# Performance work log

Measured on AMD Instinct MI355X. Metric: run time of the kernel, lower is better.

Reference implementation:

```python
import jax, jax.numpy as jnp
import numpy as np

IN_SIZE = 1024
HID = 2048
OUT = 1024
M_STEPS = 100   # max extra ponder steps -> up to M_STEPS+1 total steps
EPS = 0.01


def setup_inputs() -> dict:
    key = jax.random.key(0)
    ks = jax.random.split(key, 11)
    inv = 1.0 / np.sqrt(HID)

    def unif(k, shape, scale):
        return jax.random.uniform(k, shape, jnp.float32, -scale, scale)

    return {
        "x": jax.random.normal(ks[0], (IN_SIZE,), jnp.float32),
        "h0": jax.random.normal(ks[1], (HID,), jnp.float32) * 0.1,
        "c0": jax.random.normal(ks[2], (HID,), jnp.float32) * 0.1,
        "W_ih": unif(ks[3], (4 * HID, 1 + IN_SIZE), inv),
        "b_ih": unif(ks[4], (4 * HID,), inv),
        "W_hh": unif(ks[5], (4 * HID, HID), inv),
        "b_hh": unif(ks[6], (4 * HID,), inv),
        "w_halt": unif(ks[7], (HID,), inv),
        "b_halt": jnp.ones((1,), jnp.float32),  # fc_halt.bias = 1.0 per source
        "W_out": unif(ks[8], (OUT, HID), inv),
        "b_out": unif(ks[9], (OUT,), inv),
    }


def reference(x, h0, c0, W_ih, b_ih, W_hh, b_hh, w_halt, b_halt, W_out, b_out):
    # Input contribution is constant across steps except the prepended halt flag
    # (1 on first step, 0 after). Precompute it once.
    ih_x = W_ih[:, 1:] @ x + b_ih + b_hh      # (4H,)
    w_flag = W_ih[:, 0]                        # (4H,)

    def step(carry, flag):
        h, c = carry
        gates = ih_x + flag * w_flag + W_hh @ h  # (4H,)
        i, f, g, o = jnp.split(gates, 4)
        i = jax.nn.sigmoid(i)
        f = jax.nn.sigmoid(f)
        g = jnp.tanh(g)
        o = jax.nn.sigmoid(o)
        c = f * c + i * g
        h = o * jnp.tanh(c)
        return (h, c), (h, c)

    flags = jnp.concatenate(
        [jnp.ones((1,), x.dtype), jnp.zeros((M_STEPS,), x.dtype)])
    _, (H, C) = jax.lax.scan(step, (h0, c0), flags)  # (M+1, HID) each

    p = jax.nn.sigmoid(H @ w_halt + b_halt[0])       # (M+1,) halting probs
    csum = jnp.cumsum(p)
    halted = csum >= 1.0 - EPS
    # n = first step where cumulative halt prob crosses threshold, capped at M
    n = jnp.where(jnp.any(halted), jnp.argmax(halted), M_STEPS)
    # remainder r = 1 - sum(p[:n]); csum[n] - p[n] == sum(p[:n])
    r = 1.0 - jnp.where(n > 0, csum[n] - p[n], 0.0)

    idx = jnp.arange(M_STEPS + 1)
    w = jnp.where(idx < n, p, jnp.where(idx == n, r, 0.0))  # (M+1,)

    outputs = H @ W_out.T + b_out                    # (M+1, OUT)
    output = w @ outputs                             # (OUT,) weights sum to 1
    h_out = w @ H                                    # (HID,)
    c_out = w @ C                                    # (HID,)
    ponder = n.astype(x.dtype) + 1.0 + r
    return output, (h_out, c_out), ponder
```

## Files before the change

kernel.cpp:

```cpp
#include <hip/hip_runtime.h>


#define HID    2048
#define INS    1024
#define OUTS   1024
#define MSTEPS 100
#define NBLK   256
#define NTHR   512
#define NWAVE  8
#define JPB    8
#define RPB    32
#define SLOTF  16

typedef unsigned long long u64;
typedef unsigned int u32;

__device__ __forceinline__ float wave_allreduce(float v) {
    #pragma unroll
    for (int off = 32; off > 0; off >>= 1)
        v += __shfl_xor(v, off, 64);
    return v;
}

__device__ __forceinline__ u32 bf16_2(float a, float b) {
    u32 ua = __float_as_uint(a), ub = __float_as_uint(b);
    ua = (ua + 0x7fffu + ((ua >> 16) & 1u)) >> 16;
    ub = (ub + 0x7fffu + ((ub >> 16) & 1u)) >> 16;
    return ua | (ub << 16);
}
__device__ __forceinline__ float blo(u32 u) { return __uint_as_float(u << 16); }
__device__ __forceinline__ float bhi(u32 u) { return __uint_as_float(u & 0xffff0000u); }

__device__ __forceinline__ u64 pack_tag(unsigned tag, float v) {
    return ((u64)tag << 32) | (u64)__float_as_uint(v);
}
__device__ __forceinline__ u64 aload(const u64* p) {
    return __hip_atomic_load(p, __ATOMIC_RELAXED, __HIP_MEMORY_SCOPE_AGENT);
}
__device__ __forceinline__ void astore(u64* p, u64 v) {
    __hip_atomic_store(p, v, __ATOMIC_RELAXED, __HIP_MEMORY_SCOPE_AGENT);
}


__global__ __launch_bounds__(NTHR, 2) void alstm_kernel(
    const float* __restrict__ x,      const float* __restrict__ h0,
    const float* __restrict__ c0,     const float* __restrict__ W_ih,
    const float* __restrict__ b_ih,   const float* __restrict__ W_hh,
    const float* __restrict__ b_hh,   const float* __restrict__ w_halt,
    const float* __restrict__ b_halt, const float* __restrict__ W_out,
    const float* __restrict__ b_out,  float* __restrict__ out,
    float* __restrict__ ws)
{
    const int b    = blockIdx.x;
    const int tid  = threadIdx.x;
    const int wave = tid >> 6;
    const int lane = tid & 63;

    float* arrive = ws;
    float* mail   = ws + NBLK * SLOTF;
    float* hbuf0  = ws + 2 * NBLK * SLOTF;
    float* hbuf1  = hbuf0 + HID;
    float* hbar_g = hbuf0 + 2 * HID;

    __shared__ u32   whh_u[RPB * 1024];
    __shared__ u32   hpk[HID / 2];
    __shared__ float x_lds[INS];
    __shared__ float hbar_lds[HID];
    __shared__ float gate_lds[RPB];
    __shared__ float ihx_lds[RPB];
    __shared__ float wflag_lds[RPB];
    __shared__ float red_lds[4];
    __shared__ float bcast_lds;
    __shared__ float psum[NWAVE];

    const float bh = b_halt[0];
    const int j_own = b * JPB + tid;

    const int lr0   = 4 * wave;
    const int rbase = (lr0 >> 3) * HID + b * JPB + (lr0 & 7);

    #define SYNC_ROUND(tag_, part_, dot_) do {                                 \
        if (tid == 0) {                                                        \
            __threadfence();           \
            astore((u64*)(arrive + SLOTF * b), pack_tag((tag_), (part_)));     \
        }                                                                      \
        if (b == 0) {                                                          \
            float pf = 0.f;                                                    \
            if (tid < NBLK) {                                                  \
                u64 v;                                                         \
                do { v = aload((u64*)(arrive + SLOTF * tid)); }                \
                while ((unsigned)(v >> 32) != (unsigned)(tag_));               \
                pf = __uint_as_float((unsigned)v);                             \
            }                                                                  \
            float s = wave_allreduce(pf);                                      \
            if (lane == 0 && wave < 4) red_lds[wave] = s;                      \
            __syncthreads();                                                   \
            if (tid == 0)                                                      \
                bcast_lds = red_lds[0] + red_lds[1] + red_lds[2] + red_lds[3]; \
            __syncthreads();                                                   \
            if (tid < NBLK)                                                    \
                astore((u64*)(mail + SLOTF * tid), pack_tag((tag_), bcast_lds)); \
        }                                                                      \
        if (tid == 0) {                                                        \
            u64 v;                                                             \
            do { v = aload((u64*)(mail + SLOTF * b)); }                        \
            while ((unsigned)(v >> 32) != (unsigned)(tag_));                   \
            bcast_lds = __uint_as_float((unsigned)v);                          \
            __threadfence();        \
        }                                                                      \
        __syncthreads();                                                       \
        (dot_) = bcast_lds;                                                    \
    } while (0)

    ((float2*)x_lds)[tid] = ((const float2*)x)[tid];
    {
        float4 v = ((const float4*)h0)[tid];
        hpk[2 * tid]     = bf16_2(v.x, v.y);
        hpk[2 * tid + 1] = bf16_2(v.z, v.w);
    }
    __syncthreads();

    {
        float4 st[4][8];
        #pragma unroll
        for (int rr = 0; rr < 4; ++rr) {
            const float4* src = (const float4*)(W_hh + (size_t)(rbase + rr) * HID);
            #pragma unroll
            for (int m = 0; m < 8; ++m) st[rr][m] = src[lane + 64 * m];
        }
        __builtin_amdgcn_sched_barrier(0);
        #pragma unroll
        for (int rr = 0; rr < 4; ++rr) {
            u32* dst = whh_u + (lr0 + rr) * (HID / 2);
            #pragma unroll
            for (int m = 0; m < 8; ++m) {
                dst[2 * (lane + 64 * m)]     = bf16_2(st[rr][m].x, st[rr][m].y);
                dst[2 * (lane + 64 * m) + 1] = bf16_2(st[rr][m].z, st[rr][m].w);
            }
        }
    }

    float a0 = 0.f, a1 = 0.f, a2 = 0.f, a3 = 0.f;
    {
        const float*  wr_[4];
        const float4* wv_[4];
        int p0_[4];
        #pragma unroll
        for (int rr = 0; rr < 4; ++rr) {
            const int lr = lr0 + rr;
            const int r  = (lr >> 3) * HID + b * JPB + (lr & 7);
            wr_[rr] = W_ih + (size_t)r * (INS + 1) + 1;
            p0_[rr] = (4 - ((r + 1) & 3)) & 3;
            wv_[rr] = (const float4*)(wr_[rr] + p0_[rr]);
        }
        float bsum = 0.f, wflg = 0.f;
        if (lane < 4) {
            const int lr = lr0 + lane;
            const int r  = (lr >> 3) * HID + b * JPB + (lr & 7);
            bsum = b_ih[r] + b_hh[r];
            wflg = W_ih[(size_t)r * (INS + 1)];
        }
        #pragma unroll
        for (int ii = 0; ii < 4; ++ii) {
            const int i = lane + 64 * ii;
            if (i < 255) {
                #pragma unroll
                for (int rr = 0; rr < 4; ++rr) {
                    float4 w4 = wv_[rr][i];
                    const int k = p0_[rr] + 4 * i;
                    float s = w4.x * x_lds[k]     + w4.y * x_lds[k + 1]
                            + w4.z * x_lds[k + 2] + w4.w * x_lds[k + 3];
                    if      (rr == 0) a0 += s;
                    else if (rr == 1) a1 += s;
                    else if (rr == 2) a2 += s;
                    else              a3 += s;
                }
            }
        }
        if (lane < 4) {
            #pragma unroll
            for (int rr = 0; rr < 4; ++rr) {
                const int p0 = p0_[rr];
                const int e  = (lane < p0) ? lane : 1020 + lane;
                float s = wr_[rr][e] * x_lds[e];
                if      (rr == 0) a0 += s;
                else if (rr == 1) a1 += s;
                else if (rr == 2) a2 += s;
                else              a3 += s;
            }
        }
        a0 = wave_allreduce(a0);
        a1 = wave_allreduce(a1);
        a2 = wave_allreduce(a2);
        a3 = wave_allreduce(a3);
        if (lane < 4) {
            float myacc = (lane == 0) ? a0 : (lane == 1) ? a1 : (lane == 2) ? a2 : a3;
            ihx_lds[lr0 + lane]   = myacc + bsum;
            wflag_lds[lr0 + lane] = wflg;
        }
    }

    float c_reg = 0.f, h_reg = 0.f, hbar = 0.f, cbar = 0.f;
    if (tid < JPB) c_reg = c0[j_own];

    float csum = 0.f, r_halt = 0.f;
    int   n_halt = 0;
    for (int t = 0; t <= MSTEPS; ++t) {
        {
            const uint4* hp = (const uint4*)hpk;
            float g0 = 0.f, g1 = 0.f, g2 = 0.f, g3 = 0.f;
            #pragma unroll
            for (int m = 0; m < 4; ++m) {
                uint4 hu = hp[lane + 64 * m];
                float h0a = blo(hu.x), h1a = bhi(hu.x);
                float h2a = blo(hu.y), h3a = bhi(hu.y);
                float h4a = blo(hu.z), h5a = bhi(hu.z);
                float h6a = blo(hu.w), h7a = bhi(hu.w);
                #pragma unroll
                for (int rr = 0; rr < 4; ++rr) {
                    const uint4* wp = (const uint4*)(whh_u + (lr0 + rr) * (HID / 2));
                    uint4 wu = wp[lane + 64 * m];
                    float s = blo(wu.x) * h0a + bhi(wu.x) * h1a
                            + blo(wu.y) * h2a + bhi(wu.y) * h3a
                            + blo(wu.z) * h4a + bhi(wu.z) * h5a
                            + blo(wu.w) * h6a + bhi(wu.w) * h7a;
                    if      (rr == 0) g0 += s;
                    else if (rr == 1) g1 += s;
                    else if (rr == 2) g2 += s;
                    else              g3 += s;
                }
            }
            g0 = wave_allreduce(g0);
            g1 = wave_allreduce(g1);
            g2 = wave_allreduce(g2);
            g3 = wave_allreduce(g3);
            if (lane < 4) {
                float myacc = (lane == 0) ? g0 : (lane == 1) ? g1 : (lane == 2) ? g2 : g3;
                float bb = ihx_lds[lr0 + lane];
                if (t == 0) bb += wflag_lds[lr0 + lane];
                gate_lds[lr0 + lane] = bb + myacc;
            }
        }
        __syncthreads();

        float part = 0.f;
        float* hdst = (t & 1) ? hbuf1 : hbuf0;
        if (tid < JPB) {
            float iv = gate_lds[0 * JPB + tid];
            float fv = gate_lds[1 * JPB + tid];
            float gv = gate_lds[2 * JPB + tid];
            float ov = gate_lds[3 * JPB + tid];
            iv = 1.f / (1.f + expf(-iv));
            fv = 1.f / (1.f + expf(-fv));
            gv = tanhf(gv);
            ov = 1.f / (1.f + expf(-ov));
            c_reg = fv * c_reg + iv * gv;
            h_reg = ov * tanhf(c_reg);
            hdst[j_own] = h_reg;
            part = h_reg * w_halt[j_own];
        }
        part += __shfl_down(part, 4, 64);
        part += __shfl_down(part, 2, 64);
        part += __shfl_down(part, 1, 64);

        float dotv;
        SYNC_ROUND(t + 1, part, dotv);

        float p = 1.f / (1.f + expf(-(dotv + bh)));
        float prev = csum;
        csum += p;
        bool halt_now = (csum >= 1.f - 0.01f) || (t == MSTEPS);
        float wt = halt_now ? (1.f - prev) : p;
        if (tid < JPB) { hbar += wt * h_reg; cbar += wt * c_reg; }
        if (halt_now) { n_halt = t; r_halt = 1.f - prev; break; }

        {
            float4 v = ((const float4*)hdst)[tid];
            hpk[2 * tid]     = bf16_2(v.x, v.y);
            hpk[2 * tid + 1] = bf16_2(v.z, v.w);
        }
        __syncthreads();
    }

    if (tid < JPB) {
        out[OUTS + j_own]       = hbar;
        out[OUTS + HID + j_own] = cbar;
        hbar_g[j_own] = hbar;
    }
    if (b == 0 && tid == 0) out[OUTS + 2 * HID] = (float)(n_halt + 1) + r_halt;

    float dummy;
    SYNC_ROUND(n_halt + 2, 0.f, dummy);
    (void)dummy;

    __syncthreads();
    ((float4*)hbar_lds)[tid] = ((const float4*)hbar_g)[tid];
    __syncthreads();

    {
        const int row  = b * 4 + (wave & 3);
        const int half = wave >> 2;
        const float4* wrow = (const float4*)(W_out + (size_t)row * HID) + half * 256;
        const float4* hv   = (const float4*)hbar_lds + half * 256;
        float acc = 0.f;
        #pragma unroll
        for (int m = 0; m < 4; ++m) {
            float4 w4 = wrow[lane + 64 * m];
            float4 h4 = hv[lane + 64 * m];
            acc += w4.x * h4.x + w4.y * h4.y + w4.z * h4.z + w4.w * h4.w;
        }
        acc = wave_allreduce(acc);
        if (lane == 0) psum[wave] = acc;
    }
    __syncthreads();
    if (tid < 4) {
        int row = b * 4 + tid;
        out[row] = psum[tid] + psum[tid + 4] + b_out[row];
    }
    #undef SYNC_ROUND
}

extern "C" void kernel_launch(void* const* d_in, const int* in_sizes, int n_in,
                              void* d_out, int out_size, void* d_ws, size_t ws_size,
                              hipStream_t stream) {
    const float* x      = (const float*)d_in[0];
    const float* h0     = (const float*)d_in[1];
    const float* c0     = (const float*)d_in[2];
    const float* W_ih   = (const float*)d_in[3];
    const float* b_ih   = (const float*)d_in[4];
    const float* W_hh   = (const float*)d_in[5];
    const float* b_hh   = (const float*)d_in[6];
    const float* w_halt = (const float*)d_in[7];
    const float* b_halt = (const float*)d_in[8];
    const float* W_out  = (const float*)d_in[9];
    const float* b_out  = (const float*)d_in[10];
    float* out = (float*)d_out;
    float* ws  = (float*)d_ws;

    hipMemsetAsync(d_ws, 0, 32768, stream);

    alstm_kernel<<<dim3(NBLK), dim3(NTHR), 0, stream>>>(
        x, h0, c0, W_ih, b_ih, W_hh, b_hh, w_halt, b_halt, W_out, b_out,
        out, ws);
}
```

Baseline: 175.3 us.

## Overlap weight staging with first step, accumulate full hbar locally, drop final grid sync

Restructures the persistent LSTM kernel in four ways. The W_hh staging loads are double-buffered and the first-step gate matvec is computed in fp32 while converting to bf16. Every block now accumulates the full weighted h in LDS from the shared h buffer, so the final grid-wide sync round and the global hbar round trip disappear. W_out, W_ih and the small vectors are prefetched into registers at kernel start, and the spin-waits gain s_sleep backoff. This adds register pressure and an extra per-step LDS read-modify-write, and the sleep may add latency to each barrier.

```diff
diff --git a/kernel.cpp b/kernel.cpp
--- a/kernel.cpp
+++ b/kernel.cpp
@@ -60,22 +60,18 @@
     float* mail   = ws + NBLK * SLOTF;
     float* hbuf0  = ws + 2 * NBLK * SLOTF;
     float* hbuf1  = hbuf0 + HID;
-    float* hbar_g = hbuf0 + 2 * HID;
 
     __shared__ u32   whh_u[RPB * 1024];
     __shared__ u32   hpk[HID / 2];
     __shared__ float x_lds[INS];
-    __shared__ float hbar_lds[HID];
+    __shared__ float hjoint[HID];
     __shared__ float gate_lds[RPB];
     __shared__ float ihx_lds[RPB];
-    __shared__ float wflag_lds[RPB];
     __shared__ float red_lds[4];
     __shared__ float bcast_lds;
     __shared__ float psum[NWAVE];
 
-    const float bh = b_halt[0];
     const int j_own = b * JPB + tid;
-
     const int lr0   = 4 * wave;
     const int rbase = (lr0 >> 3) * HID + b * JPB + (lr0 & 7);
 
@@ -87,9 +83,11 @@
         if (b == 0) {                                                          \
             float pf = 0.f;                                                    \
             if (tid < NBLK) {                                                  \
-                u64 v;                                                         \
-                do { v = aload((u64*)(arrive + SLOTF * tid)); }                \
-                while ((unsigned)(v >> 32) != (unsigned)(tag_));               \
+                u64 v = aload((u64*)(arrive + SLOTF * tid));                   \
+                while ((unsigned)(v >> 32) != (unsigned)(tag_)) {              \
+                    __builtin_amdgcn_s_sleep(1);                               \
+                    v = aload((u64*)(arrive + SLOTF * tid));                   \
+                }                                                              \
                 pf = __uint_as_float((unsigned)v);                             \
             }                                                                  \
             float s = wave_allreduce(pf);                                      \
@@ -102,9 +100,11 @@
                 astore((u64*)(mail + SLOTF * tid), pack_tag((tag_), bcast_lds)); \
         }                                                                      \
         if (tid == 0) {                                                        \
-            u64 v;                                                             \
-            do { v = aload((u64*)(mail + SLOTF * b)); }                        \
-            while ((unsigned)(v >> 32) != (unsigned)(tag_));                   \
+            u64 v = aload((u64*)(mail + SLOTF * b));                           \
+            while ((unsigned)(v >> 32) != (unsigned)(tag_)) {                  \
+                __builtin_amdgcn_s_sleep(1);                                   \
+                v = aload((u64*)(mail + SLOTF * b));                           \
+            }                                                                  \
             bcast_lds = __uint_as_float((unsigned)v);                          \
             __threadfence();        \
         }                                                                      \
@@ -112,103 +112,177 @@
         (dot_) = bcast_lds;                                                    \
     } while (0)
 
-    ((float2*)x_lds)[tid] = ((const float2*)x)[tid];
-    {
-        float4 v = ((const float4*)h0)[tid];
-        hpk[2 * tid]     = bf16_2(v.x, v.y);
-        hpk[2 * tid + 1] = bf16_2(v.z, v.w);
-    }
+    #define ISSUE_ROW(BUF, RR) do {                                           \
+        const float4* src_ = (const float4*)(W_hh + (size_t)(rbase + (RR)) * HID); \
+        _Pragma("unroll")                                                      \
+        for (int m = 0; m < 8; ++m) BUF[m] = src_[lane + 64 * m];              \
+    } while (0)
+
+    #define CONVROW(BUF, RR, GACC) do {                                       \
+        u32* dst_ = whh_u + (lr0 + (RR)) * (HID / 2);                         \
+        const float4* h4_ = (const float4*)hjoint;                            \
+        _Pragma("unroll")                                                      \
+        for (int m = 0; m < 8; ++m) {                                         \
+            float4 w4 = BUF[m];                                               \
+            dst_[2 * (lane + 64 * m)]     = bf16_2(w4.x, w4.y);               \
+            dst_[2 * (lane + 64 * m) + 1] = bf16_2(w4.z, w4.w);               \
+            float4 hv_ = h4_[lane + 64 * m];                                  \
+            GACC += w4.x * hv_.x + w4.y * hv_.y + w4.z * hv_.z + w4.w * hv_.w;\
+        }                                                                      \
+    } while (0)
+
+    const float bh = b_halt[0];
+    float2 xv  = ((const float2*)x)[tid];
+    float4 h0v = ((const float4*)h0)[tid];
+    float c_reg = (tid < JPB) ? c0[j_own]     : 0.f;
+    float whv   = (tid < JPB) ? w_halt[j_own] : 0.f;
+    float bo    = (tid < 4)   ? b_out[b * 4 + tid] : 0.f;
+    float bsum = 0.f, wflg = 0.f;
+    if (lane < 4) {
+        const int lr = lr0 + lane;
+        const int r  = (lr >> 3) * HID + b * JPB + (lr & 7);
+        bsum = b_ih[r] + b_hh[r];
+        wflg = W_ih[(size_t)r * (INS + 1)];
+    }
+    __builtin_amdgcn_sched_barrier(0);
+
+    const int orow = b * 4 + (wave & 3);
+    const int ohalf = wave >> 2;
+    const float4* wrow = (const float4*)(W_out + (size_t)orow * HID) + ohalf * 256;
+    float4 wo0 = wrow[lane], wo1 = wrow[lane + 64],
+           wo2 = wrow[lane + 128], wo3 = wrow[lane + 192];
+
+    const float*  wr_[4];
+    const float4* wv_[4];
+    int p0_[4];
+    #pragma unroll
+    for (int rr = 0; rr < 4; ++rr) {
+        const int lr = lr0 + rr;
+        const int r  = (lr >> 3) * HID + b * JPB + (lr & 7);
+        wr_[rr] = W_ih + (size_t)r * (INS + 1) + 1;
+        p0_[rr] = (4 - ((r + 1) & 3)) & 3;
+        wv_[rr] = (const float4*)(wr_[rr] + p0_[rr]);
+    }
+    float4 iw0[4], iw1[4], iw2[4], iw3[4];
+    #pragma unroll
+    for (int ii = 0; ii < 4; ++ii) {
+        const int i  = lane + 64 * ii;
+        const int ic = (i < 255) ? i : 0;
+        iw0[ii] = wv_[0][ic];
+        iw1[ii] = wv_[1][ic];
+        iw2[ii] = wv_[2][ic];
+        iw3[ii] = wv_[3][ic];
+    }
+
+    float4 wa[8], wb[8];
+    ISSUE_ROW(wa, 0);
+    ISSUE_ROW(wb, 1);
+    __builtin_amdgcn_sched_barrier(0);
+
+    ((float2*)x_lds)[tid]  = xv;
+    ((float4*)hjoint)[tid] = h0v;
     __syncthreads();
 
-    {
-        float4 st[4][8];
+    float a0 = 0.f, a1 = 0.f, a2 = 0.f, a3 = 0.f;
+    #pragma unroll
+    for (int ii = 0; ii < 4; ++ii) {
+        const int   i   = lane + 64 * ii;
+        const int   ic  = (i < 255) ? i : 0;
+        const float msk = (i < 255) ? 1.f : 0.f;
         #pragma unroll
         for (int rr = 0; rr < 4; ++rr) {
-            const float4* src = (const float4*)(W_hh + (size_t)(rbase + rr) * HID);
-            #pragma unroll
-            for (int m = 0; m < 8; ++m) st[rr][m] = src[lane + 64 * m];
+            float4 w4 = (rr == 0) ? iw0[ii] : (rr == 1) ? iw1[ii]
+                      : (rr == 2) ? iw2[ii] : iw3[ii];
+            const int k = p0_[rr] + 4 * ic;
+            float s = w4.x * x_lds[k]     + w4.y * x_lds[k + 1]
+                    + w4.z * x_lds[k + 2] + w4.w * x_lds[k + 3];
+            s *= msk;
+            if      (rr == 0) a0 += s;
+            else if (rr == 1) a1 += s;
+            else if (rr == 2) a2 += s;
+            else              a3 += s;
         }
-        __builtin_amdgcn_sched_barrier(0);
+    }
+    if (lane < 4) {
         #pragma unroll
         for (int rr = 0; rr < 4; ++rr) {
-            u32* dst = whh_u + (lr0 + rr) * (HID / 2);
-            #pragma unroll
-            for (int m = 0; m < 8; ++m) {
-                dst[2 * (lane + 64 * m)]     = bf16_2(st[rr][m].x, st[rr][m].y);
-                dst[2 * (lane + 64 * m) + 1] = bf16_2(st[rr][m].z, st[rr][m].w);
-            }
+            const int p0 = p0_[rr];
+            const int e  = (lane < p0) ? lane : 1020 + lane;
+            float s = wr_[rr][e] * x_lds[e];
+            if      (rr == 0) a0 += s;
+            else if (rr == 1) a1 += s;
+            else if (rr == 2) a2 += s;
+            else              a3 += s;
         }
     }
 
-    float a0 = 0.f, a1 = 0.f, a2 = 0.f, a3 = 0.f;
-    {
-        const float*  wr_[4];
-        const float4* wv_[4];
-        int p0_[4];
-        #pragma unroll
-        for (int rr = 0; rr < 4; ++rr) {
-            const int lr = lr0 + rr;
-            const int r  = (lr >> 3) * HID + b * JPB + (lr & 7);
-            wr_[rr] = W_ih + (size_t)r * (INS + 1) + 1;
-            p0_[rr] = (4 - ((r + 1) & 3)) & 3;
-            wv_[rr] = (const float4*)(wr_[rr] + p0_[rr]);
-        }
-        float bsum = 0.f, wflg = 0.f;
-        if (lane < 4) {
-            const int lr = lr0 + lane;
-            const int r  = (lr >> 3) * HID + b * JPB + (lr & 7);
-            bsum = b_ih[r] + b_hh[r];
-            wflg = W_ih[(size_t)r * (INS + 1)];
-        }
-        #pragma unroll
-        for (int ii = 0; ii < 4; ++ii) {
-            const int i = lane + 64 * ii;
-            if (i < 255) {
-                #pragma unroll
-                for (int rr = 0; rr < 4; ++rr) {
-                    float4 w4 = wv_[rr][i];
-                    const int k = p0_[rr] + 4 * i;
-                    float s = w4.x * x_lds[k]     + w4.y * x_lds[k + 1]
-                            + w4.z * x_lds[k + 2] + w4.w * x_lds[k + 3];
-                    if      (rr == 0) a0 += s;
-                    else if (rr == 1) a1 += s;
-                    else if (rr == 2) a2 += s;
-                    else              a3 += s;
-                }
-            }
-        }
-        if (lane < 4) {
-            #pragma unroll
-            for (int rr = 0; rr < 4; ++rr) {
-                const int p0 = p0_[rr];
-                const int e  = (lane < p0) ? lane : 1020 + lane;
-                float s = wr_[rr][e] * x_lds[e];
-                if      (rr == 0) a0 += s;
-                else if (rr == 1) a1 += s;
-                else if (rr == 2) a2 += s;
-                else              a3 += s;
-            }
-        }
-        a0 = wave_allreduce(a0);
-        a1 = wave_allreduce(a1);
-        a2 = wave_allreduce(a2);
-        a3 = wave_allreduce(a3);
-        if (lane < 4) {
-            float myacc = (lane == 0) ? a0 : (lane == 1) ? a1 : (lane == 2) ? a2 : a3;
-            ihx_lds[lr0 + lane]   = myacc + bsum;
-            wflag_lds[lr0 + lane] = wflg;
-        }
-    }
-
-    float c_reg = 0.f, h_reg = 0.f, hbar = 0.f, cbar = 0.f;
-    if (tid < JPB) c_reg = c0[j_own];
-
+    float g0 = 0.f, g1 = 0.f, g2 = 0.f, g3 = 0.f;
+    CONVROW(wa, 0, g0);  ISSUE_ROW(wa, 2);
+    CONVROW(wb, 1, g1);  ISSUE_ROW(wb, 3);
+    CONVROW(wa, 2, g2);
+    CONVROW(wb, 3, g3);
+
+    a0 = wave_allreduce(a0); a1 = wave_allreduce(a1);
+    a2 = wave_allreduce(a2); a3 = wave_allreduce(a3);
+    g0 = wave_allreduce(g0); g1 = wave_allreduce(g1);
+    g2 = wave_allreduce(g2); g3 = wave_allreduce(g3);
+    if (lane < 4) {
+        float av = (lane == 0) ? a0 : (lane == 1) ? a1 : (lane == 2) ? a2 : a3;
+        float gv = (lane == 0) ? g0 : (lane == 1) ? g1 : (lane == 2) ? g2 : g3;
+        ihx_lds[lr0 + lane]  = av + bsum;
+        gate_lds[lr0 + lane] = av + bsum + wflg + gv;
+    }
+    __syncthreads();
+    ((float4*)hjoint)[tid] = make_float4(0.f, 0.f, 0.f, 0.f);
+
+    float h_reg = 0.f, cbar = 0.f;
     float csum = 0.f, r_halt = 0.f;
     int   n_halt = 0;
     for (int t = 0; t <= MSTEPS; ++t) {
+        float part = 0.f;
+        float* hdst = (t & 1) ? hbuf1 : hbuf0;
+        if (tid < JPB) {
+            float iv = gate_lds[0 * JPB + tid];
+            float fv = gate_lds[1 * JPB + tid];
+            float gv = gate_lds[2 * JPB + tid];
+            float ov = gate_lds[3 * JPB + tid];
+            iv = 1.f / (1.f + expf(-iv));
+            fv = 1.f / (1.f + expf(-fv));
+            gv = tanhf(gv);
+            ov = 1.f / (1.f + expf(-ov));
+            c_reg = fv * c_reg + iv * gv;
+            h_reg = ov * tanhf(c_reg);
+            hdst[j_own] = h_reg;
+            part = h_reg * whv;
+        }
+        part += __shfl_down(part, 4, 64);
+        part += __shfl_down(part, 2, 64);
+        part += __shfl_down(part, 1, 64);
+
+        float dotv;
+        SYNC_ROUND(t + 1, part, dotv);
+
+        float p = 1.f / (1.f + expf(-(dotv + bh)));
+        float prev = csum;
+        csum += p;
+        bool  halt_now = (csum >= 1.f - 0.01f) || (t == MSTEPS);
+        float wt = halt_now ? (1.f - prev) : p;
+
+        float4 hv = ((const float4*)hdst)[tid];
+        float4 hb = ((float4*)hjoint)[tid];
+        hb.x += wt * hv.x; hb.y += wt * hv.y;
+        hb.z += wt * hv.z; hb.w += wt * hv.w;
+        ((float4*)hjoint)[tid] = hb;
+        if (tid < JPB) cbar += wt * c_reg;
+        if (halt_now) { n_halt = t; r_halt = 1.f - prev; break; }
+
+        hpk[2 * tid]     = bf16_2(hv.x, hv.y);
+        hpk[2 * tid + 1] = bf16_2(hv.z, hv.w);
+        __syncthreads();
+
         {
             const uint4* hp = (const uint4*)hpk;
-            float g0 = 0.f, g1 = 0.f, g2 = 0.f, g3 = 0.f;
+            float m0 = 0.f, m1 = 0.f, m2 = 0.f, m3 = 0.f;
             #pragma unroll
             for (int m = 0; m < 4; ++m) {
                 uint4 hu = hp[lane + 64 * m];
@@ -224,100 +298,46 @@
                             + blo(wu.y) * h2a + bhi(wu.y) * h3a
                             + blo(wu.z) * h4a + bhi(wu.z) * h5a
                             + blo(wu.w) * h6a + bhi(wu.w) * h7a;
-                    if      (rr == 0) g0 += s;
-                    else if (rr == 1) g1 += s;
-                    else if (rr == 2) g2 += s;
-                    else              g3 += s;
+                    if      (rr == 0) m0 += s;
+                    else if (rr == 1) m1 += s;
+                    else if (rr == 2) m2 += s;
+                    else              m3 += s;
                 }
             }
-            g0 = wave_allreduce(g0);
-            g1 = wave_allreduce(g1);
-            g2 = wave_allreduce(g2);
-            g3 = wave_allreduce(g3);
+            m0 = wave_allreduce(m0); m1 = wave_allreduce(m1);
+            m2 = wave_allreduce(m2); m3 = wave_allreduce(m3);
             if (lane < 4) {
-                float myacc = (lane == 0) ? g0 : (lane == 1) ? g1 : (lane == 2) ? g2 : g3;
-                float bb = ihx_lds[lr0 + lane];
-                if (t == 0) bb += wflag_lds[lr0 + lane];
-                gate_lds[lr0 + lane] = bb + myacc;
+                float mv = (lane == 0) ? m0 : (lane == 1) ? m1
+                         : (lane == 2) ? m2 : m3;
+                gate_lds[lr0 + lane] = ihx_lds[lr0 + lane] + mv;
             }
         }
         __syncthreads();
-
-        float part = 0.f;
-        float* hdst = (t & 1) ? hbuf1 : hbuf0;
-        if (tid < JPB) {
-            float iv = gate_lds[0 * JPB + tid];
-            float fv = gate_lds[1 * JPB + tid];
-            float gv = gate_lds[2 * JPB + tid];
-            float ov = gate_lds[3 * JPB + tid];
-            iv = 1.f / (1.f + expf(-iv));
-            fv = 1.f / (1.f + expf(-fv));
-            gv = tanhf(gv);
-            ov = 1.f / (1.f + expf(-ov));
-            c_reg = fv * c_reg + iv * gv;
-            h_reg = ov * tanhf(c_reg);
-            hdst[j_own] = h_reg;
-            part = h_reg * w_halt[j_own];
-        }
-        part += __shfl_down(part, 4, 64);
-        part += __shfl_down(part, 2, 64);
-        part += __shfl_down(part, 1, 64);
-
-        float dotv;
-        SYNC_ROUND(t + 1, part, dotv);
-
-        float p = 1.f / (1.f + expf(-(dotv + bh)));
-        float prev = csum;
-        csum += p;
-        bool halt_now = (csum >= 1.f - 0.01f) || (t == MSTEPS);
-        float wt = halt_now ? (1.f - prev) : p;
-        if (tid < JPB) { hbar += wt * h_reg; cbar += wt * c_reg; }
-        if (halt_now) { n_halt = t; r_halt = 1.f - prev; break; }
-
-        {
-            float4 v = ((const float4*)hdst)[tid];
-            hpk[2 * tid]     = bf16_2(v.x, v.y);
-            hpk[2 * tid + 1] = bf16_2(v.z, v.w);
-        }
-        __syncthreads();
-    }
-
+    }
+
+    __syncthreads();
     if (tid < JPB) {
-        out[OUTS + j_own]       = hbar;
+        out[OUTS + j_own]       = hjoint[j_own];
         out[OUTS + HID + j_own] = cbar;
-        hbar_g[j_own] = hbar;
     }
     if (b == 0 && tid == 0) out[OUTS + 2 * HID] = (float)(n_halt + 1) + r_halt;
 
-    float dummy;
-    SYNC_ROUND(n_halt + 2, 0.f, dummy);
-    (void)dummy;
-
-    __syncthreads();
-    ((float4*)hbar_lds)[tid] = ((const float4*)hbar_g)[tid];
-    __syncthreads();
-
     {
-        const int row  = b * 4 + (wave & 3);
-        const int half = wave >> 2;
-        const float4* wrow = (const float4*)(W_out + (size_t)row * HID) + half * 256;
-        const float4* hv   = (const float4*)hbar_lds + half * 256;
+        const float4* hb4 = (const float4*)hjoint + ohalf * 256;
         float acc = 0.f;
-        #pragma unroll
-        for (int m = 0; m < 4; ++m) {
-            float4 w4 = wrow[lane + 64 * m];
-            float4 h4 = hv[lane + 64 * m];
-            acc += w4.x * h4.x + w4.y * h4.y + w4.z * h4.z + w4.w * h4.w;
-        }
+        { float4 h4 = hb4[lane];       acc += wo0.x*h4.x + wo0.y*h4.y + wo0.z*h4.z + wo0.w*h4.w; }
+        { float4 h4 = hb4[lane + 64];  acc += wo1.x*h4.x + wo1.y*h4.y + wo1.z*h4.z + wo1.w*h4.w; }
+        { float4 h4 = hb4[lane + 128]; acc += wo2.x*h4.x + wo2.y*h4.y + wo2.z*h4.z + wo2.w*h4.w; }
+        { float4 h4 = hb4[lane + 192]; acc += wo3.x*h4.x + wo3.y*h4.y + wo3.z*h4.z + wo3.w*h4.w; }
         acc = wave_allreduce(acc);
         if (lane == 0) psum[wave] = acc;
     }
     __syncthreads();
-    if (tid < 4) {
-        int row = b * 4 + tid;
-        out[row] = psum[tid] + psum[tid + 4] + b_out[row];
-    }
+    if (tid < 4) out[b * 4 + tid] = psum[tid] + psum[tid + 4] + bo;
+
     #undef SYNC_ROUND
+    #undef ISSUE_ROW
+    #undef CONVROW
 }
 
 extern "C" void kernel_launch(void* const* d_in, const int* in_sizes, int n_in,
```

Result: faster. 168.7 us (-3.8%).
